# Kernel optimization log

Measured on AMD Instinct MI355X. Metric: run time of the kernel, lower is better.

The kernel has to match this reference:

```python
import jax, jax.numpy as jnp
import numpy as np

NUM_EXPERTS = 8
TOP_K = 2


def setup_inputs() -> dict:
    key = jax.random.key(0)
    ks = jax.random.split(key, 6)
    D, H, E = 1024, 4096, NUM_EXPERTS
    B, S = 4, 2048
    s = 0.02
    return {
        "x": jax.random.normal(ks[0], (B, S, D), jnp.float32),
        "scale_embeddings": jax.random.normal(ks[1], (10, D), jnp.float32) * s,
        "router_w": jax.random.normal(ks[2], (E, D), jnp.float32) * s,
        "router_b": jnp.zeros((E,), jnp.float32),
        "fc1_w": jax.random.normal(ks[3], (E, H, D), jnp.float32) * s,
        "fc1_b": jnp.zeros((E, H), jnp.float32),
        "fc2_w": jax.random.normal(ks[4], (E, D, H), jnp.float32) * s,
        "fc2_b": jnp.zeros((E, D), jnp.float32),
        "scale_idx": 3,
    }


def reference(x, scale_embeddings, router_w, router_b, fc1_w, fc1_b, fc2_w, fc2_b, scale_idx):
    B, S, D = x.shape
    T = B * S
    # Scale-aware router (eval mode: no jitter, temperature=1.0).
    xs = x + scale_embeddings[scale_idx][None, None, :]
    logits = jnp.einsum('bsd,ed->bse', xs, router_w) + router_b  # [B,S,E]
    top_w, top_idx = jax.lax.top_k(logits, TOP_K)                 # [B,S,K]
    top_w = jax.nn.softmax(top_w, axis=-1)

    # Dense per-expert FFN (tanh-approx GELU), then gather top-k expert outputs.
    xf = x.reshape(T, D)
    outs = []
    for e in range(NUM_EXPERTS):
        h = jax.nn.gelu(xf @ fc1_w[e].T + fc1_b[e], approximate=True)  # [T,H]
        outs.append(h @ fc2_w[e].T + fc2_b[e])                          # [T,D]
    all_out = jnp.stack(outs)                                           # [E,T,D]

    idx_f = top_idx.reshape(T, TOP_K)
    w_f = top_w.reshape(T, TOP_K)
    gathered = all_out[idx_f, jnp.arange(T)[:, None]]  # [T,K,D]
    out = (gathered * w_f[..., None]).sum(axis=1)      # [T,D]
    return out.reshape(B, S, D)
```

## Files before the change

kernel.cpp:

```cpp
#include <hip/hip_runtime.h>
#include <math.h>

#define TTOK 8192
#define DDIM 1024
#define HDIM 4096
#define NEXP 8
#define NASSIGN (TTOK * 2)

typedef float f32x4 __attribute__((ext_vector_type(4)));
typedef short s16x8 __attribute__((ext_vector_type(8)));

__device__ __forceinline__ unsigned short f2bf(float f) {
  union { float f; unsigned int u; } v; v.f = f;
  unsigned int u = v.u;
  u += 0x7FFFu + ((u >> 16) & 1u);
  return (unsigned short)(u >> 16);
}

__device__ __forceinline__ float gelu_fast(float x) {
  float u = 0.7978845608028654f * x * (1.0f + 0.044715f * x * x);
  return x / (1.0f + __expf(-2.0f * u));
}

__global__ void cvt_bf16_k(const float* __restrict__ src,
                           unsigned short* __restrict__ dst, int n4) {
  int i = blockIdx.x * blockDim.x + threadIdx.x;
  if (i >= n4) return;
  float4 v = ((const float4*)src)[i];
  ushort4 o;
  o.x = f2bf(v.x); o.y = f2bf(v.y); o.z = f2bf(v.z); o.w = f2bf(v.w);
  ((ushort4*)dst)[i] = o;
}

__global__ void router_k(const float* __restrict__ x, const float* __restrict__ se,
                         const int* __restrict__ sidx, const float* __restrict__ rw,
                         const float* __restrict__ rb,
                         int* __restrict__ e0, int* __restrict__ e1,
                         float* __restrict__ w0, float* __restrict__ w1,
                         int* __restrict__ counts) {
  int t = blockIdx.x * 4 + (threadIdx.x >> 6);
  int lane = threadIdx.x & 63;
  const float4* xp = (const float4*)(x + (size_t)t * DDIM) + lane * 4;
  const float4* sp = (const float4*)(se + (size_t)sidx[0] * DDIM) + lane * 4;
  float xs[16];
#pragma unroll
  for (int c = 0; c < 4; ++c) {
    float4 a = xp[c], b = sp[c];
    xs[c * 4 + 0] = a.x + b.x; xs[c * 4 + 1] = a.y + b.y;
    xs[c * 4 + 2] = a.z + b.z; xs[c * 4 + 3] = a.w + b.w;
  }
  double acc[NEXP];
#pragma unroll
  for (int e = 0; e < NEXP; ++e) acc[e] = 0.0;
#pragma unroll
  for (int e = 0; e < NEXP; ++e) {
    const float4* wp = (const float4*)(rw + (size_t)e * DDIM) + lane * 4;
#pragma unroll
    for (int c = 0; c < 4; ++c) {
      float4 wv = wp[c];
      acc[e] += (double)xs[c * 4 + 0] * wv.x + (double)xs[c * 4 + 1] * wv.y +
                (double)xs[c * 4 + 2] * wv.z + (double)xs[c * 4 + 3] * wv.w;
    }
  }
#pragma unroll
  for (int e = 0; e < NEXP; ++e) {
#pragma unroll
    for (int m = 32; m >= 1; m >>= 1) acc[e] += __shfl_xor(acc[e], m, 64);
  }
  if (lane == 0) {
    float lg[NEXP];
    for (int e = 0; e < NEXP; ++e) lg[e] = (float)acc[e] + rb[e];
    int i0 = 0; float l0 = lg[0];
    for (int e = 1; e < NEXP; ++e) if (lg[e] > l0) { l0 = lg[e]; i0 = e; }
    int i1 = -1; float l1 = -1e30f;
    for (int e = 0; e < NEXP; ++e) if (e != i0 && lg[e] > l1) { l1 = lg[e]; i1 = e; }
    float z = expf(l1 - l0);
    float p0 = 1.0f / (1.0f + z);
    e0[t] = i0; e1[t] = i1; w0[t] = p0; w1[t] = 1.0f - p0;
    atomicAdd(&counts[i0], 1);
    atomicAdd(&counts[i1], 1);
  }
}

__global__ void scan_k(const int* __restrict__ counts, int* __restrict__ offsets,
                       int* __restrict__ cursors, int4* __restrict__ tileT,
                       int* __restrict__ ntiles) {
  if (threadIdx.x == 0 && blockIdx.x == 0) {
    int s = 0;
    for (int e = 0; e < NEXP; ++e) { offsets[e] = s; cursors[e] = s; s += counts[e]; }
    offsets[NEXP] = s;
    int nt = 0;
    for (int e = 0; e < NEXP; ++e)
      for (int m0 = offsets[e]; m0 < offsets[e + 1]; m0 += 128)
        tileT[nt++] = make_int4(m0, offsets[e + 1], e, 0);
    ntiles[0] = nt;
  }
}

__global__ void scatter_k(const int* __restrict__ e0, const int* __restrict__ e1,
                          const float* __restrict__ w0, const float* __restrict__ w1,
                          int* __restrict__ cursors, int* __restrict__ buckets,
                          float* __restrict__ wts, int* __restrict__ s0,
                          int* __restrict__ s1) {
  int t = blockIdx.x * blockDim.x + threadIdx.x;
  if (t >= TTOK) return;
  int a = e0[t];
  int p = atomicAdd(&cursors[a], 1);
  buckets[p] = t; wts[p] = w0[t]; s0[t] = p;
  a = e1[t];
  p = atomicAdd(&cursors[a], 1);
  buckets[p] = t; wts[p] = w1[t]; s1[t] = p;
}

__global__ void gather_k(const float* __restrict__ x, const int* __restrict__ buckets,
                         unsigned short* __restrict__ Xg) {
  int r = blockIdx.x;
  int t = buckets[r];
  int i = threadIdx.x;
  float4 v = ((const float4*)(x + (size_t)t * DDIM))[i];
  ushort4 o;
  o.x = f2bf(v.x); o.y = f2bf(v.y); o.z = f2bf(v.z); o.w = f2bf(v.w);
  ((ushort4*)(Xg + (size_t)r * DDIM))[i] = o;
}

template <int KD, int ND, int EPI>
__global__ __launch_bounds__(256) void moe_gemm_k(
    const unsigned short* __restrict__ A,
    const unsigned short* __restrict__ W,
    const float* __restrict__ bias,
    const int4* __restrict__ tileT, const int* __restrict__ ntiles,
    unsigned short* __restrict__ Hout, float* __restrict__ Yout) {
  constexpr int NT = ND / 128;
  __shared__ unsigned short As[128 * 64];
  __shared__ unsigned short Bs[128 * 64];

  const int tid = threadIdx.x;
  const int lane = tid & 63;
  const int w = tid >> 6;
  const int q = lane >> 4;
  const int c16 = lane & 15;
  const int cx = lane & 7;
  const int wrow = (w >> 1) * 64;
  const int wcol = (w & 1) * 64;
  const int srow = w * 8 + (lane >> 3);
  const int swz = (lane & 7) ^ (lane >> 3);

  const int total = ntiles[0] * NT;

  for (int tt = blockIdx.x; tt < total; tt += gridDim.x) {
    const int mt = tt / NT;
    const int nb = tt - mt * NT;
    const int4 tl = tileT[mt];
    const int m0 = tl.x, row1 = tl.y, e = tl.z;
    const int n0 = nb * 128;
    const unsigned short* We = W + (size_t)e * ND * KD;

    f32x4 acc[4][4];
#pragma unroll
    for (int i = 0; i < 4; ++i)
#pragma unroll
      for (int j = 0; j < 4; ++j) acc[i][j] = {0.f, 0.f, 0.f, 0.f};

    for (int kt = 0; kt < KD / 64; ++kt) {
      const int k0 = kt * 64;
      __syncthreads();
#pragma unroll
      for (int i = 0; i < 4; ++i) {
        int ar = m0 + i * 32 + srow;
        if (ar > row1 - 1) ar = row1 - 1;
        const unsigned short* ga = A + (size_t)ar * KD + k0 + swz * 8;
        __builtin_amdgcn_global_load_lds(
            (const __attribute__((address_space(1))) void*)ga,
            (__attribute__((address_space(3))) void*)(As + (i * 32 + w * 8) * 64),
            16, 0, 0);
      }
#pragma unroll
      for (int i = 0; i < 4; ++i) {
        int br = n0 + i * 32 + srow;
        const unsigned short* gb = We + (size_t)br * KD + k0 + swz * 8;
        __builtin_amdgcn_global_load_lds(
            (const __attribute__((address_space(1))) void*)gb,
            (__attribute__((address_space(3))) void*)(Bs + (i * 32 + w * 8) * 64),
            16, 0, 0);
      }
      __syncthreads();
#pragma unroll
      for (int ks = 0; ks < 2; ++ks) {
        s16x8 af[4], bfr[4];
#pragma unroll
        for (int i = 0; i < 4; ++i)
          af[i] = *((const s16x8*)(As + (wrow + i * 16 + c16) * 64 +
                                   (((ks * 4 + q) ^ cx) * 8)));
#pragma unroll
        for (int j = 0; j < 4; ++j)
          bfr[j] = *((const s16x8*)(Bs + (wcol + j * 16 + c16) * 64 +
                                    (((ks * 4 + q) ^ cx) * 8)));
#pragma unroll
        for (int i = 0; i < 4; ++i)
#pragma unroll
          for (int j = 0; j < 4; ++j)
            acc[i][j] = __builtin_amdgcn_mfma_f32_16x16x32_bf16(af[i], bfr[j], acc[i][j], 0, 0, 0);
      }
    }

    float bj[4];
#pragma unroll
    for (int j = 0; j < 4; ++j)
      bj[j] = bias[(size_t)e * ND + n0 + wcol + j * 16 + c16];
#pragma unroll
    for (int i = 0; i < 4; ++i) {
#pragma unroll
      for (int r = 0; r < 4; ++r) {
        const int m = m0 + wrow + i * 16 + q * 4 + r;
        if (m < row1) {
          if (EPI == 0) {
#pragma unroll
            for (int j = 0; j < 4; ++j) {
              const int n = n0 + wcol + j * 16 + c16;
              Hout[(size_t)m * ND + n] = f2bf(gelu_fast(acc[i][j][r] + bj[j]));
            }
          } else {
#pragma unroll
            for (int j = 0; j < 4; ++j) {
              const int n = n0 + wcol + j * 16 + c16;
              Yout[(size_t)m * ND + n] = acc[i][j][r] + bj[j];
            }
          }
        }
      }
    }
  }
}

__global__ void combine_k(const float* __restrict__ Yr, const int* __restrict__ s0,
                          const int* __restrict__ s1, const float* __restrict__ wts,
                          float* __restrict__ out) {
  int t = blockIdx.x;
  int i = threadIdx.x;
  int a = s0[t], b = s1[t];
  float wa = wts[a], wb = wts[b];
  float4 va = ((const float4*)(Yr + (size_t)a * DDIM))[i];
  float4 vb = ((const float4*)(Yr + (size_t)b * DDIM))[i];
  float4 o;
  o.x = wa * va.x + wb * vb.x;
  o.y = wa * va.y + wb * vb.y;
  o.z = wa * va.z + wb * vb.z;
  o.w = wa * va.w + wb * vb.w;
  ((float4*)(out + (size_t)t * DDIM))[i] = o;
}

extern "C" void kernel_launch(void* const* d_in, const int* in_sizes, int n_in,
                              void* d_out, int out_size, void* d_ws, size_t ws_size,
                              hipStream_t stream) {
  const float* x  = (const float*)d_in[0];
  const float* se = (const float*)d_in[1];
  const float* rw = (const float*)d_in[2];
  const float* rb = (const float*)d_in[3];
  const float* w1 = (const float*)d_in[4];
  const float* b1 = (const float*)d_in[5];
  const float* w2 = (const float*)d_in[6];
  const float* b2 = (const float*)d_in[7];
  const int* sidx = (const int*)d_in[8];
  float* out = (float*)d_out;

  char* ws = (char*)d_ws;
  size_t off = 0;
  unsigned short* w1b = (unsigned short*)(ws + off); off += (size_t)NEXP * HDIM * DDIM * 2;
  unsigned short* w2b = (unsigned short*)(ws + off); off += (size_t)NEXP * DDIM * HDIM * 2;
  unsigned short* Xg  = (unsigned short*)(ws + off); off += (size_t)NASSIGN * DDIM * 2;
  unsigned short* Hb  = (unsigned short*)(ws + off); off += (size_t)NASSIGN * HDIM * 2;
  float* Yr = (float*)w1b;
  int*   counts  = (int*)(ws + off); off += 64;
  int*   offsets = (int*)(ws + off); off += 64;
  int*   cursors = (int*)(ws + off); off += 64;
  int*   ntiles  = (int*)(ws + off); off += 64;
  int*   e0  = (int*)(ws + off);   off += (size_t)TTOK * 4;
  int*   e1  = (int*)(ws + off);   off += (size_t)TTOK * 4;
  float* tw0 = (float*)(ws + off); off += (size_t)TTOK * 4;
  float* tw1 = (float*)(ws + off); off += (size_t)TTOK * 4;
  int*   s0  = (int*)(ws + off);   off += (size_t)TTOK * 4;
  int*   s1  = (int*)(ws + off);   off += (size_t)TTOK * 4;
  int*   buckets = (int*)(ws + off); off += (size_t)NASSIGN * 4;
  float* wts = (float*)(ws + off);   off += (size_t)NASSIGN * 4;
  int4*  tileT = (int4*)(ws + off);  off += 256 * 16;

  hipMemsetAsync(counts, 0, 64, stream);

  const int n4 = NEXP * HDIM * DDIM / 4;
  cvt_bf16_k<<<n4 / 256, 256, 0, stream>>>(w1, w1b, n4);
  cvt_bf16_k<<<n4 / 256, 256, 0, stream>>>(w2, w2b, n4);
  router_k<<<TTOK / 4, 256, 0, stream>>>(x, se, sidx, rw, rb, e0, e1, tw0, tw1, counts);
  scan_k<<<1, 64, 0, stream>>>(counts, offsets, cursors, tileT, ntiles);
  scatter_k<<<TTOK / 256, 256, 0, stream>>>(e0, e1, tw0, tw1, cursors, buckets, wts, s0, s1);
  gather_k<<<NASSIGN, 256, 0, stream>>>(x, buckets, Xg);

  moe_gemm_k<DDIM, HDIM, 0><<<1024, 256, 0, stream>>>(Xg, w1b, b1, tileT, ntiles, Hb, Yr);
  moe_gemm_k<HDIM, DDIM, 1><<<1024, 256, 0, stream>>>(Hb, w2b, b2, tileT, ntiles, Hb, Yr);
  combine_k<<<TTOK, 256, 0, stream>>>(Yr, s0, s1, wts, out);
}
```

Baseline: 1.149 ms.

## Map GEMM N-tiles to XCDs, hoist load addresses, merge weight conversions

The MoE GEMM tile schedule now assigns each XCD (blockIdx & 7) a fixed slice of N-column tiles, so each XCD's L2 holds a smaller weight working set. The grid grows to 2048 blocks, and per-tile A/B global pointers are computed once outside the K loop. The two fp32-to-bf16 weight conversion launches become one kernel that handles 8 elements per thread. The XCD mapping assumes round-robin block dispatch across 8 XCDs and a fixed stride of 256 per XCD, and it could unbalance work when the tile count is uneven.

```diff
diff --git a/kernel.cpp b/kernel.cpp
--- a/kernel.cpp
+++ b/kernel.cpp
@@ -22,14 +22,19 @@
   return x / (1.0f + __expf(-2.0f * u));
 }
 
-__global__ void cvt_bf16_k(const float* __restrict__ src,
-                           unsigned short* __restrict__ dst, int n4) {
+__global__ void cvt_bf16_k(const float* __restrict__ w1, unsigned short* __restrict__ w1b,
+                           const float* __restrict__ w2, unsigned short* __restrict__ w2b,
+                           int n8) {
   int i = blockIdx.x * blockDim.x + threadIdx.x;
-  if (i >= n4) return;
-  float4 v = ((const float4*)src)[i];
-  ushort4 o;
-  o.x = f2bf(v.x); o.y = f2bf(v.y); o.z = f2bf(v.z); o.w = f2bf(v.w);
-  ((ushort4*)dst)[i] = o;
+  const float* src; unsigned short* dst;
+  if (i < n8) { src = w1; dst = w1b; } else { src = w2; dst = w2b; i -= n8; }
+#pragma unroll
+  for (int c = 0; c < 2; ++c) {
+    float4 v = ((const float4*)src)[i * 2 + c];
+    ushort4 o;
+    o.x = f2bf(v.x); o.y = f2bf(v.y); o.z = f2bf(v.z); o.w = f2bf(v.w);
+    ((ushort4*)dst)[i * 2 + c] = o;
+  }
 }
 
 __global__ void router_k(const float* __restrict__ x, const float* __restrict__ se,
@@ -131,6 +136,7 @@
     const int4* __restrict__ tileT, const int* __restrict__ ntiles,
     unsigned short* __restrict__ Hout, float* __restrict__ Yout) {
   constexpr int NT = ND / 128;
+  constexpr int G = NT / 8;
   __shared__ unsigned short As[128 * 64];
   __shared__ unsigned short Bs[128 * 64];
 
@@ -145,16 +151,28 @@
   const int srow = w * 8 + (lane >> 3);
   const int swz = (lane & 7) ^ (lane >> 3);
 
-  const int total = ntiles[0] * NT;
-
-  for (int tt = blockIdx.x; tt < total; tt += gridDim.x) {
-    const int mt = tt / NT;
-    const int nb = tt - mt * NT;
+  const int xcd = blockIdx.x & 7;
+  const int lid = blockIdx.x >> 3;
+  const int bound = ntiles[0] * G;
+
+  for (int idx = lid; idx < bound; idx += 256) {
+    const int mt = idx / G;
+    const int nb = xcd * G + (idx - mt * G);
     const int4 tl = tileT[mt];
     const int m0 = tl.x, row1 = tl.y, e = tl.z;
     const int n0 = nb * 128;
     const unsigned short* We = W + (size_t)e * ND * KD;
 
+    const unsigned short* aptr[4];
+    const unsigned short* bptr[4];
+#pragma unroll
+    for (int i = 0; i < 4; ++i) {
+      int ar = m0 + i * 32 + srow;
+      if (ar > row1 - 1) ar = row1 - 1;
+      aptr[i] = A + (size_t)ar * KD + swz * 8;
+      bptr[i] = We + (size_t)(n0 + i * 32 + srow) * KD + swz * 8;
+    }
+
     f32x4 acc[4][4];
 #pragma unroll
     for (int i = 0; i < 4; ++i)
@@ -165,24 +183,17 @@
       const int k0 = kt * 64;
       __syncthreads();
 #pragma unroll
-      for (int i = 0; i < 4; ++i) {
-        int ar = m0 + i * 32 + srow;
-        if (ar > row1 - 1) ar = row1 - 1;
-        const unsigned short* ga = A + (size_t)ar * KD + k0 + swz * 8;
+      for (int i = 0; i < 4; ++i)
         __builtin_amdgcn_global_load_lds(
-            (const __attribute__((address_space(1))) void*)ga,
+            (const __attribute__((address_space(1))) void*)(aptr[i] + k0),
             (__attribute__((address_space(3))) void*)(As + (i * 32 + w * 8) * 64),
             16, 0, 0);
-      }
-#pragma unroll
-      for (int i = 0; i < 4; ++i) {
-        int br = n0 + i * 32 + srow;
-        const unsigned short* gb = We + (size_t)br * KD + k0 + swz * 8;
+#pragma unroll
+      for (int i = 0; i < 4; ++i)
         __builtin_amdgcn_global_load_lds(
-            (const __attribute__((address_space(1))) void*)gb,
+            (const __attribute__((address_space(1))) void*)(bptr[i] + k0),
             (__attribute__((address_space(3))) void*)(Bs + (i * 32 + w * 8) * 64),
             16, 0, 0);
-      }
       __syncthreads();
 #pragma unroll
       for (int ks = 0; ks < 2; ++ks) {
@@ -286,15 +297,14 @@
 
   hipMemsetAsync(counts, 0, 64, stream);
 
-  const int n4 = NEXP * HDIM * DDIM / 4;
-  cvt_bf16_k<<<n4 / 256, 256, 0, stream>>>(w1, w1b, n4);
-  cvt_bf16_k<<<n4 / 256, 256, 0, stream>>>(w2, w2b, n4);
+  const int n8 = NEXP * HDIM * DDIM / 8;
+  cvt_bf16_k<<<2 * n8 / 256, 256, 0, stream>>>(w1, w1b, w2, w2b, n8);
   router_k<<<TTOK / 4, 256, 0, stream>>>(x, se, sidx, rw, rb, e0, e1, tw0, tw1, counts);
   scan_k<<<1, 64, 0, stream>>>(counts, offsets, cursors, tileT, ntiles);
   scatter_k<<<TTOK / 256, 256, 0, stream>>>(e0, e1, tw0, tw1, cursors, buckets, wts, s0, s1);
   gather_k<<<NASSIGN, 256, 0, stream>>>(x, buckets, Xg);
 
-  moe_gemm_k<DDIM, HDIM, 0><<<1024, 256, 0, stream>>>(Xg, w1b, b1, tileT, ntiles, Hb, Yr);
-  moe_gemm_k<HDIM, DDIM, 1><<<1024, 256, 0, stream>>>(Hb, w2b, b2, tileT, ntiles, Hb, Yr);
+  moe_gemm_k<DDIM, HDIM, 0><<<2048, 256, 0, stream>>>(Xg, w1b, b1, tileT, ntiles, Hb, Yr);
+  moe_gemm_k<HDIM, DDIM, 1><<<2048, 256, 0, stream>>>(Hb, w2b, b2, tileT, ntiles, Hb, Yr);
   combine_k<<<TTOK, 256, 0, stream>>>(Yr, s0, s1, wts, out);
 }
```

After: 1.145 ms. About the same (-0.3%).
